# Kernel optimization log

Measured on AMD Instinct MI355X. Metric: run time of the kernel, lower is better.

## Reference

```python
import jax, jax.numpy as jnp
import numpy as np

INPUT_HSIZE = 40960
ACC_H = 256
HID1 = 32
HID2 = 32
OUT = 1
MAX_ACTIVE_FEATURES = 32


def setup_inputs() -> dict:
    key = jax.random.key(0)
    ks = jax.random.split(key, 12)
    B = 8192
    std = (2.0 / MAX_ACTIVE_FEATURES) ** 0.5
    inp = {
        "white_features": jax.random.uniform(ks[0], (B, INPUT_HSIZE), dtype=jnp.float32),
        "black_features": jax.random.uniform(ks[1], (B, INPUT_HSIZE), dtype=jnp.float32),
        "stm": jax.random.uniform(ks[2], (B, 1), dtype=jnp.float32),
        # feature transformer (white/black accumulator) params, torch Linear layout [out, in]
        "w_white": std * jax.random.normal(ks[3], (ACC_H, INPUT_HSIZE), dtype=jnp.float32),
        "b_white": jnp.zeros((ACC_H,), dtype=jnp.float32),
        "w_black": std * jax.random.normal(ks[4], (ACC_H, INPUT_HSIZE), dtype=jnp.float32),
        "b_black": jnp.zeros((ACC_H,), dtype=jnp.float32),
        "w1": jax.random.normal(ks[5], (HID1, 2 * ACC_H), dtype=jnp.float32) * (2.0 / (2 * ACC_H)) ** 0.5,
        "b1": jnp.zeros((HID1,), dtype=jnp.float32),
        "w2": jax.random.normal(ks[6], (HID2, HID1), dtype=jnp.float32) * (2.0 / HID1) ** 0.5,
        "b2": jnp.zeros((HID2,), dtype=jnp.float32),
        "w_out": jax.random.normal(ks[7], (OUT, HID2), dtype=jnp.float32) * (2.0 / HID2) ** 0.5,
        "b_out": jnp.zeros((OUT,), dtype=jnp.float32),
    }
    return inp


def reference(white_features, black_features, stm,
              w_white, b_white, w_black, b_black,
              w1, b1, w2, b2, w_out, b_out):
    # feature transformer: [B, INPUT_HSIZE] @ [INPUT_HSIZE, ACC_H]
    white_acc = white_features @ w_white.T + b_white  # [B, 256]
    black_acc = black_features @ w_black.T + b_black  # [B, 256]
    # stm-weighted concat: white-first when stm==0, black-first when stm==1
    acc = (1.0 - stm) * jnp.concatenate([white_acc, black_acc], axis=1) \
          + stm * jnp.concatenate([black_acc, white_acc], axis=1)  # [B, 512]
    in_1 = jnp.clip(acc, 0.0, 1.0)
    out_1 = in_1 @ w1.T + b1
    in_2 = jnp.clip(out_1, 0.0, 1.0)
    out_2 = in_2 @ w2.T + b2
    in_out = jnp.clip(out_2, 0.0, 1.0)
    out = in_out @ w_out.T + b_out  # [B, 1]
    return out
```

## Files before the change

### kernel.cpp

```cpp
#include <hip/hip_runtime.h>
#include <hip/hip_bf16.h>
#include <stdint.h>

#define K_DIM 40960
#define NROWS 8192
#define ACCH 256
#define KSPLIT 4
#define KCHUNK (K_DIM / KSPLIT)
#define BM 256
#define BK 64
#define NT (KCHUNK / BK)

typedef float f32x4 __attribute__((ext_vector_type(4)));
typedef _Float16 f16x8 __attribute__((ext_vector_type(8)));

__device__ __forceinline__ uint32_t pack2_f16(float a, float b) {
  _Float16 ha = (_Float16)a, hb = (_Float16)b;
  uint16_t ua = __builtin_bit_cast(uint16_t, ha);
  uint16_t ub = __builtin_bit_cast(uint16_t, hb);
  return (uint32_t)ua | ((uint32_t)ub << 16);
}

__device__ __forceinline__ void gload_lds16(const void* g, void* l) {
  __builtin_amdgcn_global_load_lds((const __attribute__((address_space(1))) uint32_t*)g,
                                   (__attribute__((address_space(3))) uint32_t*)l, 16, 0, 0);
}

__global__ void convert_w_kernel(const float* __restrict__ ww, const float* __restrict__ wb,
                                 uint16_t* __restrict__ dst) {
  uint32_t gid = blockIdx.x * blockDim.x + threadIdx.x;
  uint64_t e = (uint64_t)gid * 8u;
  const uint64_t half = (uint64_t)ACCH * K_DIM;
  const float* src = (e < half) ? (ww + e) : (wb + (e - half));
  float4 f0 = *(const float4*)src;
  float4 f1 = *(const float4*)(src + 4);
  uint4 o;
  o.x = pack2_f16(f0.x, f0.y);
  o.y = pack2_f16(f0.z, f0.w);
  o.z = pack2_f16(f1.x, f1.y);
  o.w = pack2_f16(f1.z, f1.w);
  *(uint4*)(dst + e) = o;
}

__global__ __launch_bounds__(512, 2) void ft_gemm(
    const float* __restrict__ featW, const float* __restrict__ featB,
    const uint16_t* __restrict__ wts, float* __restrict__ partials)
{
  extern __shared__ char smem[];
  const int tid = threadIdx.x;
  const int bid = blockIdx.x;
  const int mt  = bid >> 3;
  const int cc  = bid & 1;
  const int ksp = (bid >> 1) & 3;
  const float*    feat = cc ? featB : featW;
  const uint16_t* wp   = wts + (uint64_t)cc * ACCH * K_DIM;
  const int m0 = mt * BM;
  const int k0 = ksp * KCHUNK;

  const int wid  = tid >> 6;
  const int lane = tid & 63;
  const int wm   = wid >> 2;
  const int wn   = wid & 3;
  const int lrow = lane & 15;
  const int lk   = lane >> 4;

  const int ar0 = tid >> 3, as0 = tid & 7;
  const float* aSrc0 = feat + (uint64_t)(m0 + ar0) * K_DIM + k0 + as0 * 8;
  const int aOff0 = ar0 * 128 + ((as0 ^ (ar0 & 7)) * 16);

  const int gsegB = wid * 64 + lane;
  const int br0 = gsegB >> 3;
  const int bs0 = (gsegB & 7) ^ (br0 & 7);
  const uint16_t* bSrc0 = wp + (uint64_t)br0 * K_DIM + k0 + bs0 * 8;

  float4 av[4][2];
  auto loadA = [&]() {
    #pragma unroll
    for (int p = 0; p < 4; ++p) {
      const float* s = aSrc0 + (uint64_t)p * 64u * K_DIM;
      av[p][0] = *(const float4*)(s);
      av[p][1] = *(const float4*)(s + 4);
    }
    aSrc0 += BK;
  };
  auto writeA = [&](int buf) {
    #pragma unroll
    for (int p = 0; p < 4; ++p) {
      uint4 o;
      o.x = pack2_f16(av[p][0].x, av[p][0].y);
      o.y = pack2_f16(av[p][0].z, av[p][0].w);
      o.z = pack2_f16(av[p][1].x, av[p][1].y);
      o.w = pack2_f16(av[p][1].z, av[p][1].w);
      *(uint4*)(smem + buf * 32768 + aOff0 + p * 8192) = o;
    }
  };
  auto issueB = [&](int buf) {
    #pragma unroll
    for (int i = 0; i < 4; ++i) {
      gload_lds16(bSrc0 + (uint64_t)i * 64u * K_DIM,
                  smem + 65536 + buf * 32768 + (i * 8 + wid) * 1024);
    }
    bSrc0 += BK;
  };

  loadA();
  issueB(0);
  writeA(0);
  loadA();
  issueB(1);
  asm volatile("s_waitcnt vmcnt(12) lgkmcnt(0)" ::: "memory");
  __builtin_amdgcn_s_barrier();

  f32x4 acc[8][4];
  #pragma unroll
  for (int m = 0; m < 8; ++m)
    #pragma unroll
    for (int n = 0; n < 4; ++n)
      acc[m][n] = (f32x4){0.f, 0.f, 0.f, 0.f};

  int bcur = 0;
  for (int t = 0; t < NT; ++t) {
    const int acur = t & 1;
    const int bnx2 = (bcur >= 1) ? bcur - 1 : bcur + 2;
    if (t < NT - 2) issueB(bnx2);
    asm volatile("" ::: "memory");
    if (t < NT - 1) writeA(acur ^ 1);
    asm volatile("" ::: "memory");
    if (t < NT - 2) loadA();
    asm volatile("" ::: "memory");

    const char* Ab = smem + acur * 32768;
    const char* Bb = smem + 65536 + bcur * 32768;
    #pragma unroll
    for (int ksub = 0; ksub < 2; ++ksub) {
      f16x8 af[8], bfr[4];
      #pragma unroll
      for (int m = 0; m < 8; ++m)
        af[m] = *(const f16x8*)(Ab + (wm * 128 + m * 16 + lrow) * 128
                                   + (((ksub * 4 + lk) ^ (lrow & 7)) * 16));
      #pragma unroll
      for (int n = 0; n < 4; ++n)
        bfr[n] = *(const f16x8*)(Bb + (wn * 64 + n * 16 + lrow) * 128
                                    + (((ksub * 4 + lk) ^ (lrow & 7)) * 16));
      #pragma unroll
      for (int m = 0; m < 8; ++m)
        #pragma unroll
        for (int n = 0; n < 4; ++n)
          acc[m][n] = __builtin_amdgcn_mfma_f32_16x16x32_f16(af[m], bfr[n], acc[m][n], 0, 0, 0);
    }

    asm volatile("s_waitcnt lgkmcnt(0)" ::: "memory");
    __builtin_amdgcn_s_barrier();
    bcur = (bcur >= 2) ? 0 : bcur + 1;
  }

  float* pbase = partials + ((uint64_t)(cc * KSPLIT + ksp) * NROWS + m0) * ACCH;
  #pragma unroll
  for (int m = 0; m < 8; ++m) {
    #pragma unroll
    for (int n = 0; n < 4; ++n) {
      int row = wm * 128 + m * 16 + lk * 4;
      int col = wn * 64 + n * 16 + lrow;
      float* dst = pbase + (uint64_t)row * ACCH + col;
      dst[0]        = acc[m][n][0];
      dst[ACCH]     = acc[m][n][1];
      dst[2 * ACCH] = acc[m][n][2];
      dst[3 * ACCH] = acc[m][n][3];
    }
  }
}

__global__ __launch_bounds__(128) void tail_kernel(
    const float* __restrict__ partials, const float* __restrict__ stm,
    const float* __restrict__ bw, const float* __restrict__ bb,
    const float* __restrict__ w1, const float* __restrict__ b1,
    const float* __restrict__ w2, const float* __restrict__ b2,
    const float* __restrict__ w_out, const float* __restrict__ b_out,
    float* __restrict__ out)
{
  __shared__ float in1[16 * 513];
  __shared__ float out1c[16 * 33];
  const int t = threadIdx.x;
  const int b0 = blockIdx.x * 16;

  for (int it = 0; it < 32; ++it) {
    int item = t + it * 128;
    int jc = item & 255;
    int rr = item >> 8;
    int b  = b0 + rr;
    float wsum = bw[jc], bsum = bb[jc];
    #pragma unroll
    for (int k = 0; k < KSPLIT; ++k) {
      wsum += partials[((uint64_t)(0 * KSPLIT + k) * NROWS + b) * ACCH + jc];
      bsum += partials[((uint64_t)(1 * KSPLIT + k) * NROWS + b) * ACCH + jc];
    }
    float s = stm[b];
    float lo = (1.f - s) * wsum + s * bsum;
    float hi = (1.f - s) * bsum + s * wsum;
    in1[rr * 513 + jc]       = fminf(fmaxf(lo, 0.f), 1.f);
    in1[rr * 513 + 256 + jc] = fminf(fmaxf(hi, 0.f), 1.f);
  }
  __syncthreads();

  const int rl = t >> 3, og = t & 7;
  float a1[4] = {0.f, 0.f, 0.f, 0.f};
  for (int j = 0; j < 512; j += 4) {
    float v0 = in1[rl * 513 + j];
    float v1 = in1[rl * 513 + j + 1];
    float v2 = in1[rl * 513 + j + 2];
    float v3 = in1[rl * 513 + j + 3];
    #pragma unroll
    for (int oi = 0; oi < 4; ++oi) {
      const float4 wv = *(const float4*)(w1 + (og * 4 + oi) * 512 + j);
      a1[oi] += v0 * wv.x + v1 * wv.y + v2 * wv.z + v3 * wv.w;
    }
  }
  #pragma unroll
  for (int oi = 0; oi < 4; ++oi) {
    int o = og * 4 + oi;
    out1c[rl * 33 + o] = fminf(fmaxf(a1[oi] + b1[o], 0.f), 1.f);
  }
  __syncthreads();

  float a2[4] = {0.f, 0.f, 0.f, 0.f};
  for (int j = 0; j < 32; ++j) {
    float v = out1c[rl * 33 + j];
    #pragma unroll
    for (int oi = 0; oi < 4; ++oi) a2[oi] += v * w2[(og * 4 + oi) * 32 + j];
  }
  float p = 0.f;
  #pragma unroll
  for (int oi = 0; oi < 4; ++oi) {
    int o = og * 4 + oi;
    p += fminf(fmaxf(a2[oi] + b2[o], 0.f), 1.f) * w_out[o];
  }
  p += __shfl_xor(p, 1, 64);
  p += __shfl_xor(p, 2, 64);
  p += __shfl_xor(p, 4, 64);
  if (og == 0) out[b0 + rl] = p + b_out[0];
}

extern "C" void kernel_launch(void* const* d_in, const int* in_sizes, int n_in,
                              void* d_out, int out_size, void* d_ws, size_t ws_size,
                              hipStream_t stream) {
  (void)in_sizes; (void)n_in; (void)out_size; (void)ws_size;
  const float* wfeat   = (const float*)d_in[0];
  const float* bfeat   = (const float*)d_in[1];
  const float* stm     = (const float*)d_in[2];
  const float* w_white = (const float*)d_in[3];
  const float* b_white = (const float*)d_in[4];
  const float* w_black = (const float*)d_in[5];
  const float* b_black = (const float*)d_in[6];
  const float* w1      = (const float*)d_in[7];
  const float* b1      = (const float*)d_in[8];
  const float* w2      = (const float*)d_in[9];
  const float* b2      = (const float*)d_in[10];
  const float* w_out   = (const float*)d_in[11];
  const float* b_out   = (const float*)d_in[12];
  float* out = (float*)d_out;

  uint16_t* wf16     = (uint16_t*)d_ws;
  float*    partials = (float*)((char*)d_ws + (uint64_t)2 * ACCH * K_DIM * 2);

  convert_w_kernel<<<10240, 256, 0, stream>>>(w_white, w_black, wf16);

  (void)hipFuncSetAttribute((const void*)ft_gemm,
                            hipFuncAttributeMaxDynamicSharedMemorySize, 163840);
  ft_gemm<<<256, 512, 163840, stream>>>(wfeat, bfeat, wf16, partials);

  tail_kernel<<<512, 128, 0, stream>>>(partials, stm, b_white, b_black,
                                       w1, b1, w2, b2, w_out, b_out, out);
}
```

Baseline: 608.9 us.

## Double-buffer A register prefetch to deepen global load pipeline

```diff
diff --git a/kernel.cpp b/kernel.cpp
--- a/kernel.cpp
+++ b/kernel.cpp
@@ -73,8 +73,8 @@
   const int bs0 = (gsegB & 7) ^ (br0 & 7);
   const uint16_t* bSrc0 = wp + (uint64_t)br0 * K_DIM + k0 + bs0 * 8;
 
-  float4 av[4][2];
-  auto loadA = [&]() {
+  float4 av0[4][2], av1[4][2];
+  auto loadA = [&](float4 (&av)[4][2]) {
     #pragma unroll
     for (int p = 0; p < 4; ++p) {
       const float* s = aSrc0 + (uint64_t)p * 64u * K_DIM;
@@ -83,7 +83,7 @@
     }
     aSrc0 += BK;
   };
-  auto writeA = [&](int buf) {
+  auto writeA = [&](int buf, const float4 (&av)[4][2]) {
     #pragma unroll
     for (int p = 0; p < 4; ++p) {
       uint4 o;
@@ -103,14 +103,6 @@
     bSrc0 += BK;
   };
 
-  loadA();
-  issueB(0);
-  writeA(0);
-  loadA();
-  issueB(1);
-  asm volatile("s_waitcnt vmcnt(12) lgkmcnt(0)" ::: "memory");
-  __builtin_amdgcn_s_barrier();
-
   f32x4 acc[8][4];
   #pragma unroll
   for (int m = 0; m < 8; ++m)
@@ -118,19 +110,7 @@
     for (int n = 0; n < 4; ++n)
       acc[m][n] = (f32x4){0.f, 0.f, 0.f, 0.f};
 
-  int bcur = 0;
-  for (int t = 0; t < NT; ++t) {
-    const int acur = t & 1;
-    const int bnx2 = (bcur >= 1) ? bcur - 1 : bcur + 2;
-    if (t < NT - 2) issueB(bnx2);
-    asm volatile("" ::: "memory");
-    if (t < NT - 1) writeA(acur ^ 1);
-    asm volatile("" ::: "memory");
-    if (t < NT - 2) loadA();
-    asm volatile("" ::: "memory");
-
-    const char* Ab = smem + acur * 32768;
-    const char* Bb = smem + 65536 + bcur * 32768;
+  auto mfma_step = [&](const char* Ab, const char* Bb) {
     #pragma unroll
     for (int ksub = 0; ksub < 2; ++ksub) {
       f16x8 af[8], bfr[4];
@@ -148,10 +128,49 @@
         for (int n = 0; n < 4; ++n)
           acc[m][n] = __builtin_amdgcn_mfma_f32_16x16x32_f16(af[m], bfr[n], acc[m][n], 0, 0, 0);
     }
-
-    asm volatile("s_waitcnt lgkmcnt(0)" ::: "memory");
-    __builtin_amdgcn_s_barrier();
-    bcur = (bcur >= 2) ? 0 : bcur + 1;
+  };
+
+  loadA(av0);
+  issueB(0);
+  writeA(0, av0);
+  loadA(av1);
+  issueB(1);
+  loadA(av0);
+  asm volatile("s_waitcnt vmcnt(20) lgkmcnt(0)" ::: "memory");
+  __builtin_amdgcn_s_barrier();
+
+  int bcur = 0;
+  for (int tt = 0; tt < NT; tt += 2) {
+    {
+      const int t = tt;
+      const int bn2 = (bcur >= 1) ? bcur - 1 : bcur + 2;
+      if (t < NT - 2) issueB(bn2);
+      asm volatile("" ::: "memory");
+      if (t < NT - 1) writeA(1, av1);
+      asm volatile("" ::: "memory");
+      if (t < NT - 3) loadA(av1);
+      asm volatile("" ::: "memory");
+      mfma_step(smem, smem + 65536 + bcur * 32768);
+      if (t < NT - 3) asm volatile("s_waitcnt vmcnt(20) lgkmcnt(0)" ::: "memory");
+      else            asm volatile("s_waitcnt vmcnt(0) lgkmcnt(0)" ::: "memory");
+      __builtin_amdgcn_s_barrier();
+    }
+    {
+      const int t = tt + 1;
+      const int b1 = (bcur >= 2) ? bcur - 2 : bcur + 1;
+      if (t < NT - 2) issueB(bcur);
+      asm volatile("" ::: "memory");
+      if (t < NT - 1) writeA(0, av0);
+      asm volatile("" ::: "memory");
+      if (t < NT - 3) loadA(av0);
+      asm volatile("" ::: "memory");
+      mfma_step(smem + 32768, smem + 65536 + b1 * 32768);
+      if (t < NT - 3)       asm volatile("s_waitcnt vmcnt(20) lgkmcnt(0)" ::: "memory");
+      else if (t == NT - 3) asm volatile("s_waitcnt vmcnt(12) lgkmcnt(0)" ::: "memory");
+      else                  asm volatile("s_waitcnt vmcnt(0) lgkmcnt(0)" ::: "memory");
+      __builtin_amdgcn_s_barrier();
+      bcur = (bcur >= 1) ? bcur - 1 : bcur + 2;
+    }
   }
 
   float* pbase = partials + ((uint64_t)(cc * KSPLIT + ksp) * NROWS + m0) * ACCH;
```

After: 1.075 ms. 1.77x slower.
